# Performance work log

Measured on AMD Instinct MI355X. Metric: run time of the kernel, lower is better.

## Reference

```python
import math
import jax, jax.numpy as jnp
import numpy as np

NLAT, NLON = 61, 120
C, H = 64, 4
DH = C // H
HID = 128
NSEG = NLAT * NLON  # number of grid points / softmax segments
EPS = 1e-6
SCALE = 1.0 / math.sqrt(DH)


def _build_geometry():
    """Neighbor pairs within theta_cutoff on the equiangular (pole-including) grid.

    The neighborhood structure is longitude-shift invariant, so we enumerate it
    for output longitude 0 and replicate with a modular longitude shift.
    """
    nlat, nlon = NLAT, NLON
    theta = np.pi * np.arange(nlat) / (nlat - 1)           # colatitudes incl. poles
    lam = 2.0 * np.pi * np.arange(nlon) / nlon
    theta_cutoff = 7.0 / math.sqrt(math.pi) * math.pi / (nlat - 1)
    ct, st = np.cos(theta), np.sin(theta)
    # great-circle distance between (theta_o, 0) and (theta_i, dlon): [nlat, nlat, nlon]
    cosd = (ct[:, None, None] * ct[None, :, None]
            + st[:, None, None] * st[None, :, None] * np.cos(lam)[None, None, :])
    dist = np.arccos(np.clip(cosd, -1.0, 1.0))
    ho, hi, dl = np.nonzero(dist <= theta_cutoff)          # E reference-column entries
    wo = np.arange(nlon)
    out_idx = (ho[:, None] * nlon + wo[None, :]).reshape(-1).astype(np.int32)
    in_idx = (hi[:, None] * nlon + (dl[:, None] + wo[None, :]) % nlon).reshape(-1).astype(np.int32)
    # quadrature (integration) weights: sin(theta) measure, zero at the poles
    w = (st * (np.pi / (nlat - 1)) * (2.0 * np.pi / nlon)).astype(np.float32)
    quad_w = np.repeat(w, nlon)                            # [NSEG]
    return jnp.asarray(out_idx), jnp.asarray(in_idx), jnp.asarray(quad_w)


def setup_inputs() -> dict:
    key = jax.random.key(0)
    ks = jax.random.split(key, 8)
    out_idx, in_idx, quad_w = _build_geometry()

    def w(k, shape, fan_in):
        return jax.random.normal(k, shape, dtype=jnp.float32) / np.float32(np.sqrt(fan_in))

    return {
        "x": jax.random.normal(ks[0], (1, C, NLAT, NLON), dtype=jnp.float32),
        "wq": w(ks[1], (C, C), C),
        "wk": w(ks[2], (C, C), C),
        "wv": w(ks[3], (C, C), C),
        "wo": w(ks[4], (C, C), C),
        "w1": w(ks[5], (HID, C), C),
        "b1": jnp.zeros((HID,), jnp.float32),
        "w2": w(ks[6], (C, HID), HID),
        "b2": jnp.zeros((C,), jnp.float32),
        "ln0_g": jnp.ones((C,), jnp.float32),
        "ln0_b": jnp.zeros((C,), jnp.float32),
        "ln1_g": jnp.ones((C,), jnp.float32),
        "ln1_b": jnp.zeros((C,), jnp.float32),
        "quad_w": quad_w,
        "out_idx": out_idx,
        "in_idx": in_idx,
    }


def _layernorm(x, g, b):
    # channel-wise LayerNorm at every spatial location; x: [B, C, H, W]
    m = jnp.mean(x, axis=1, keepdims=True)
    v = jnp.mean((x - m) ** 2, axis=1, keepdims=True)
    xh = (x - m) * jax.lax.rsqrt(v + EPS)
    return xh * g[None, :, None, None] + b[None, :, None, None]


def _neighborhood_attn(x, wq, wk, wv, wo, quad_w, out_idx, in_idx):
    # x: [B, C, nlat, nlon] (fp32)
    B = x.shape[0]
    q = jnp.einsum('oc,bchw->bohw', wq, x).reshape(B, H, DH, NSEG)
    k = jnp.einsum('oc,bchw->bohw', wk, x).reshape(B, H, DH, NSEG)
    v = jnp.einsum('oc,bchw->bohw', wv, x).reshape(B, H, DH, NSEG)
    qg = q[..., out_idx]                                   # [B,H,DH,NNZ]
    kg = k[..., in_idx]
    s = jnp.einsum('bhdn,bhdn->bhn', qg, kg) * SCALE       # [B,H,NNZ]
    s = jnp.moveaxis(s, -1, 0)                             # [NNZ,B,H]
    smax = jax.ops.segment_max(s, out_idx, num_segments=NSEG)
    # quadrature-weighted, numerically stable softmax over each neighborhood
    alpha = jnp.exp(s - smax[out_idx]) * quad_w[in_idx][:, None, None]
    vg = jnp.moveaxis(v[..., in_idx], -1, 0)               # [NNZ,B,H,DH]
    num = jax.ops.segment_sum(alpha[..., None] * vg, out_idx, num_segments=NSEG)
    den = jax.ops.segment_sum(alpha, out_idx, num_segments=NSEG)
    att = num / den[..., None]                             # [NSEG,B,H,DH]
    att = jnp.moveaxis(att, 0, -1).reshape(B, C, NLAT, NLON)
    return jnp.einsum('oc,bchw->bohw', wo, att)


def reference(x, wq, wk, wv, wo, w1, b1, w2, b2, ln0_g, ln0_b, ln1_g, ln1_b,
              quad_w, out_idx, in_idx):
    residual = x
    h0 = _layernorm(x, ln0_g, ln0_b)
    a = _neighborhood_attn(h0.astype(jnp.float32), wq, wk, wv, wo,
                           quad_w, out_idx, in_idx).astype(x.dtype)
    x1 = a + residual
    h1 = _layernorm(x1, ln1_g, ln1_b)
    m = jax.nn.gelu(jnp.einsum('fc,bchw->bfhw', w1, h1) + b1[None, :, None, None],
                    approximate=False)
    m = jnp.einsum('cf,bfhw->bchw', w2, m) + b2[None, :, None, None]
    return m + x1
```

## Files before the change

### kernel.cpp

```cpp
#include <hip/hip_runtime.h>
#include <math.h>

#define NSEG 7320
#define NLON 120
#define HIDN 128
#define ECH  16
#define MAXCH 48

__global__ __launch_bounds__(64) void k1_ln_qkv(
    const float* __restrict__ x,  const float* __restrict__ wq,
    const float* __restrict__ wk, const float* __restrict__ wv,
    const float* __restrict__ g,  const float* __restrict__ b,
    const int* __restrict__ out_idx, const int* __restrict__ in_idx,
    const float* __restrict__ qw, int E,
    float* __restrict__ q_pl, float* __restrict__ k_pl, float* __restrict__ v_pl,
    int* __restrict__ row_start, int4* __restrict__ meta,
    float4* __restrict__ zbase)
{
    const int lane = threadIdx.x;
    const int tile = blockIdx.x;
    const int grp  = blockIdx.y;

    if (grp >= 25) {
        const int n4 = (68 * NSEG) / 4;
        for (int i = ((grp - 25) * 115 + tile) * 64 + lane; i < n4; i += 2 * 115 * 64)
            zbase[i] = make_float4(0.f, 0.f, 0.f, 0.f);
        return;
    }
    if (grp == 24) {
        for (int e = tile * 64 + lane; e < E; e += 115 * 64) {
            int ho = out_idx[e * NLON] / NLON;
            if (e == 0) {
                row_start[ho] = 0;
            } else {
                int hp = out_idx[(e - 1) * NLON] / NLON;
                if (hp != ho) row_start[ho] = e;
            }
            if (e == E - 1) row_start[ho + 1] = E;
            int i0 = in_idx[e * NLON];
            int hi = i0 / NLON;
            int dl = i0 - hi * NLON;
            meta[e] = make_int4(hi * NLON, dl, __float_as_int(qw[i0]), ho);
        }
        return;
    }

    const int n = tile * 64 + lane;
    if (n >= NSEG) return;

    float xv[64];
    float s = 0.f, s2 = 0.f;
#pragma unroll
    for (int c = 0; c < 64; ++c) { float t = x[c * NSEG + n]; xv[c] = t; s += t; s2 += t * t; }
    float mean = s * 0.015625f;
    float var  = s2 * 0.015625f - mean * mean;
    float rstd = rsqrtf(var + 1e-6f);
#pragma unroll
    for (int c = 0; c < 64; ++c) xv[c] = (xv[c] - mean) * rstd * g[c] + b[c];

    const int mm    = grp >> 3;
    const int obase = (grp & 7) * 8;
    const float* __restrict__ w = (mm == 0) ? wq : (mm == 1) ? wk : wv;
    float* __restrict__ dst = (mm == 0) ? q_pl : (mm == 1) ? k_pl : v_pl;
    const float scale = (mm == 0) ? 0.25f : 1.0f;

#pragma unroll
    for (int j = 0; j < 8; ++j) {
        int o = obase + j;
        float acc = 0.f;
#pragma unroll
        for (int c = 0; c < 64; ++c) acc += w[o * 64 + c] * xv[c];
        dst[o * NSEG + n] = acc * scale;
    }
}

__global__ __launch_bounds__(128) void k2_attn(
    const float* __restrict__ q_pl, const float* __restrict__ k_pl,
    const float* __restrict__ v_pl,
    const int4* __restrict__ meta,  const int* __restrict__ row_start,
    float* __restrict__ num, float* __restrict__ den)
{
    const int id   = blockIdx.x;
    const int ho   = (id & 7) + 8 * ((id >> 3) & 7);
    if (ho >= 61) return;
    const int ch   = id >> 6;
    const int head = ch & 3;
    const int cb   = head * 16;

    const int wo  = threadIdx.x;
    const bool aw = wo < NLON;
    const int woc = aw ? wo : (NLON - 1);

    int e0 = __builtin_amdgcn_readfirstlane(row_start[ho]);
    int e1 = __builtin_amdgcn_readfirstlane(row_start[ho + 1]);
    int eb = e0 + (ch >> 2) * ECH;
    if (eb >= e1) return;
    int ee = eb + ECH; if (ee > e1) ee = e1;

    const int segc = ho * NLON + woc;
    const float* __restrict__ qb = q_pl + (size_t)cb * NSEG;
    const float* __restrict__ kb = k_pl + (size_t)cb * NSEG;
    const float* __restrict__ vb = v_pl + (size_t)cb * NSEG;

    float qreg[16];
#pragma unroll
    for (int c = 0; c < 16; ++c) qreg[c] = qb[c * NSEG + segc];

    float acc[16];
#pragma unroll
    for (int c = 0; c < 16; ++c) acc[c] = 0.f;
    float dh = 0.f;

#pragma unroll 2
    for (int e = eb; e < ee; ++e) {
        int4 mt = meta[e];
        int dlw = mt.y + woc; if (dlw >= NLON) dlw -= NLON;
        const float* __restrict__ kp = kb + (mt.x + dlw);
        const float* __restrict__ vp = vb + (mt.x + dlw);

        float sa = 0.f, sb = 0.f;
#pragma unroll
        for (int c = 0; c < 8; ++c)  sa += qreg[c]     * kp[c * NSEG];
#pragma unroll
        for (int c = 0; c < 8; ++c)  sb += qreg[8 + c] * kp[(8 + c) * NSEG];

        float qwv = aw ? __int_as_float(mt.z) : 0.f;
        float a = __expf(sa + sb) * qwv;
        dh += a;

#pragma unroll
        for (int c = 0; c < 16; ++c) acc[c] = fmaf(a, vp[c * NSEG], acc[c]);
    }

    if (aw) {
        const int seg = ho * NLON + wo;
#pragma unroll
        for (int c = 0; c < 16; ++c) atomicAdd(&num[(cb + c) * NSEG + seg], acc[c]);
        atomicAdd(&den[head * NSEG + seg], dh);
    }
}

__global__ __launch_bounds__(64) void k23a_wo_mlp1(
    const float* __restrict__ num, const float* __restrict__ den,
    const float* __restrict__ wo,  const float* __restrict__ x,
    const float* __restrict__ w1,  const float* __restrict__ b1,
    const float* __restrict__ g1,  const float* __restrict__ bb1,
    float* __restrict__ x1, float* __restrict__ m_act)
{
    const int lane = threadIdx.x;
    const int n    = blockIdx.x * 64 + lane;
    if (n >= NSEG) return;

    float rdh[4];
#pragma unroll
    for (int h = 0; h < 4; ++h) rdh[h] = 1.0f / den[h * NSEG + n];

    float x1v[64];
#pragma unroll
    for (int o = 0; o < 64; ++o) x1v[o] = x[o * NSEG + n];

    for (int c = 0; c < 64; ++c) {
        float att = num[c * NSEG + n] * rdh[c >> 4];
        const float* __restrict__ wcol = wo + c;
#pragma unroll
        for (int o = 0; o < 64; ++o) x1v[o] = fmaf(wcol[o * 64], att, x1v[o]);
    }

    if (blockIdx.y == 0) {
#pragma unroll
        for (int o = 0; o < 64; ++o) x1[o * NSEG + n] = x1v[o];
    }

    float s = 0.f, s2 = 0.f;
#pragma unroll
    for (int o = 0; o < 64; ++o) { s += x1v[o]; s2 += x1v[o] * x1v[o]; }
    float mean = s * 0.015625f;
    float var  = s2 * 0.015625f - mean * mean;
    float rstd = rsqrtf(var + 1e-6f);

    const int h0 = blockIdx.y * 16;
    float mh[16];
#pragma unroll
    for (int j = 0; j < 16; ++j) mh[j] = b1[h0 + j];
    for (int c = 0; c < 64; ++c) {
        float xn = (x1v[c] - mean) * rstd * g1[c] + bb1[c];
        const float* __restrict__ w1c = w1 + h0 * 64 + c;
#pragma unroll
        for (int j = 0; j < 16; ++j) mh[j] = fmaf(w1c[j * 64], xn, mh[j]);
    }
#pragma unroll
    for (int j = 0; j < 16; ++j)
        m_act[(h0 + j) * NSEG + n] =
            0.5f * mh[j] * (1.0f + erff(mh[j] * 0.70710678118654752f));
}

__global__ __launch_bounds__(64) void k3b_mlp2(
    const float* __restrict__ m_act, const float* __restrict__ w2,
    const float* __restrict__ b2,    const float* __restrict__ x1,
    float* __restrict__ out)
{
    const int lane = threadIdx.x;
    const int n    = blockIdx.x * 64 + lane;
    if (n >= NSEG) return;
    const int c0   = blockIdx.y * 8;

    float acc[8];
#pragma unroll
    for (int j = 0; j < 8; ++j) acc[j] = 0.f;

#pragma unroll 8
    for (int h = 0; h < HIDN; ++h) {
        float mh = m_act[h * NSEG + n];
#pragma unroll
        for (int j = 0; j < 8; ++j) acc[j] += w2[(c0 + j) * HIDN + h] * mh;
    }
#pragma unroll
    for (int j = 0; j < 8; ++j) {
        int c = c0 + j;
        out[c * NSEG + n] = acc[j] + b2[c] + x1[c * NSEG + n];
    }
}

extern "C" void kernel_launch(void* const* d_in, const int* in_sizes, int n_in,
                              void* d_out, int out_size, void* d_ws, size_t ws_size,
                              hipStream_t stream)
{
    const float* x    = (const float*)d_in[0];
    const float* wq   = (const float*)d_in[1];
    const float* wk   = (const float*)d_in[2];
    const float* wv   = (const float*)d_in[3];
    const float* wo   = (const float*)d_in[4];
    const float* w1   = (const float*)d_in[5];
    const float* b1   = (const float*)d_in[6];
    const float* w2   = (const float*)d_in[7];
    const float* b2   = (const float*)d_in[8];
    const float* ln0g = (const float*)d_in[9];
    const float* ln0b = (const float*)d_in[10];
    const float* ln1g = (const float*)d_in[11];
    const float* ln1b = (const float*)d_in[12];
    const float* qw   = (const float*)d_in[13];
    const int* out_idx = (const int*)d_in[14];
    const int* in_idx  = (const int*)d_in[15];
    float* out = (float*)d_out;

    const int NNZ = in_sizes[15];
    const int E   = NNZ / NLON;
    const size_t N64 = (size_t)NSEG * 64;

    float* ws    = (float*)d_ws;
    float* q_pl  = ws;
    float* k_pl  = ws + N64;
    float* v_pl  = ws + 2 * N64;
    float* num   = ws + 3 * N64;
    float* den   = ws + 4 * N64;
    float* x1    = ws + 4 * N64 + 4 * NSEG;
    float* m_act = ws + 5 * N64 + 4 * NSEG;
    int*   row_start = (int*)(ws + 7 * N64 + 4 * NSEG);
    int4*  meta  = (int4*)(ws + 7 * N64 + 4 * NSEG + 64);

    hipLaunchKernelGGL(k1_ln_qkv, dim3(115, 27), dim3(64), 0, stream,
                       x, wq, wk, wv, ln0g, ln0b, out_idx, in_idx, qw, E,
                       q_pl, k_pl, v_pl, row_start, meta, (float4*)num);
    hipLaunchKernelGGL(k2_attn, dim3(64 * 192), dim3(128), 0, stream,
                       q_pl, k_pl, v_pl, meta, row_start, num, den);
    hipLaunchKernelGGL(k23a_wo_mlp1, dim3(115, 8), dim3(64), 0, stream,
                       num, den, wo, x, w1, b1, ln1g, ln1b, x1, m_act);
    hipLaunchKernelGGL(k3b_mlp2, dim3(115, 8), dim3(64), 0, stream,
                       m_act, w2, b2, x1, out);
}
```

Baseline: 227.2 us.

## Fuse all stages into one cooperative persistent kernel with grid syncs

Replaces the four separate launches with a single cooperative kernel of 512 blocks × 256 threads. The stages (LN+QKV, attention, output projection, LN1+MLP1, MLP2) are separated by grid.sync, and each stage walks its work items in a grid-stride loop. The output projection is split out of MLP1 into its own phase, so LN1 now re-reads x1 from memory for each hidden group. The aim is to remove inter-kernel launch gaps, at the cost of grid-wide barriers and much lower resident occupancy for the latency-bound gather-heavy attention phase.

```diff
diff --git a/kernel.cpp b/kernel.cpp
--- a/kernel.cpp
+++ b/kernel.cpp
@@ -1,223 +1,221 @@
 #include <hip/hip_runtime.h>
+#include <hip/hip_cooperative_groups.h>
 #include <math.h>
+
+namespace cg = cooperative_groups;
 
 #define NSEG 7320
 #define NLON 120
 #define HIDN 128
 #define ECH  16
-#define MAXCH 48
-
-__global__ __launch_bounds__(64) void k1_ln_qkv(
-    const float* __restrict__ x,  const float* __restrict__ wq,
-    const float* __restrict__ wk, const float* __restrict__ wv,
-    const float* __restrict__ g,  const float* __restrict__ b,
+#define NRCH 48
+#define NTILE 29
+
+__global__ __launch_bounds__(256, 2) void mega(
+    const float* __restrict__ x,
+    const float* __restrict__ wq, const float* __restrict__ wk,
+    const float* __restrict__ wv, const float* __restrict__ wo,
+    const float* __restrict__ w1, const float* __restrict__ b1,
+    const float* __restrict__ w2, const float* __restrict__ b2,
+    const float* __restrict__ ln0g, const float* __restrict__ ln0b,
+    const float* __restrict__ ln1g, const float* __restrict__ ln1b,
+    const float* __restrict__ qw,
     const int* __restrict__ out_idx, const int* __restrict__ in_idx,
-    const float* __restrict__ qw, int E,
+    int E,
     float* __restrict__ q_pl, float* __restrict__ k_pl, float* __restrict__ v_pl,
+    float* __restrict__ num,  float* __restrict__ den,
+    float* __restrict__ x1,   float* __restrict__ m_act,
     int* __restrict__ row_start, int4* __restrict__ meta,
-    float4* __restrict__ zbase)
-{
-    const int lane = threadIdx.x;
-    const int tile = blockIdx.x;
-    const int grp  = blockIdx.y;
-
-    if (grp >= 25) {
-        const int n4 = (68 * NSEG) / 4;
-        for (int i = ((grp - 25) * 115 + tile) * 64 + lane; i < n4; i += 2 * 115 * 64)
-            zbase[i] = make_float4(0.f, 0.f, 0.f, 0.f);
-        return;
-    }
-    if (grp == 24) {
-        for (int e = tile * 64 + lane; e < E; e += 115 * 64) {
-            int ho = out_idx[e * NLON] / NLON;
-            if (e == 0) {
-                row_start[ho] = 0;
-            } else {
-                int hp = out_idx[(e - 1) * NLON] / NLON;
-                if (hp != ho) row_start[ho] = e;
-            }
-            if (e == E - 1) row_start[ho + 1] = E;
-            int i0 = in_idx[e * NLON];
-            int hi = i0 / NLON;
-            int dl = i0 - hi * NLON;
-            meta[e] = make_int4(hi * NLON, dl, __float_as_int(qw[i0]), ho);
-        }
-        return;
-    }
-
-    const int n = tile * 64 + lane;
-    if (n >= NSEG) return;
-
-    float xv[64];
-    float s = 0.f, s2 = 0.f;
-#pragma unroll
-    for (int c = 0; c < 64; ++c) { float t = x[c * NSEG + n]; xv[c] = t; s += t; s2 += t * t; }
-    float mean = s * 0.015625f;
-    float var  = s2 * 0.015625f - mean * mean;
-    float rstd = rsqrtf(var + 1e-6f);
-#pragma unroll
-    for (int c = 0; c < 64; ++c) xv[c] = (xv[c] - mean) * rstd * g[c] + b[c];
-
-    const int mm    = grp >> 3;
-    const int obase = (grp & 7) * 8;
-    const float* __restrict__ w = (mm == 0) ? wq : (mm == 1) ? wk : wv;
-    float* __restrict__ dst = (mm == 0) ? q_pl : (mm == 1) ? k_pl : v_pl;
-    const float scale = (mm == 0) ? 0.25f : 1.0f;
-
-#pragma unroll
-    for (int j = 0; j < 8; ++j) {
-        int o = obase + j;
-        float acc = 0.f;
-#pragma unroll
-        for (int c = 0; c < 64; ++c) acc += w[o * 64 + c] * xv[c];
-        dst[o * NSEG + n] = acc * scale;
-    }
-}
-
-__global__ __launch_bounds__(128) void k2_attn(
-    const float* __restrict__ q_pl, const float* __restrict__ k_pl,
-    const float* __restrict__ v_pl,
-    const int4* __restrict__ meta,  const int* __restrict__ row_start,
-    float* __restrict__ num, float* __restrict__ den)
-{
-    const int id   = blockIdx.x;
-    const int ho   = (id & 7) + 8 * ((id >> 3) & 7);
-    if (ho >= 61) return;
-    const int ch   = id >> 6;
-    const int head = ch & 3;
-    const int cb   = head * 16;
-
-    const int wo  = threadIdx.x;
-    const bool aw = wo < NLON;
-    const int woc = aw ? wo : (NLON - 1);
-
-    int e0 = __builtin_amdgcn_readfirstlane(row_start[ho]);
-    int e1 = __builtin_amdgcn_readfirstlane(row_start[ho + 1]);
-    int eb = e0 + (ch >> 2) * ECH;
-    if (eb >= e1) return;
-    int ee = eb + ECH; if (ee > e1) ee = e1;
-
-    const int segc = ho * NLON + woc;
-    const float* __restrict__ qb = q_pl + (size_t)cb * NSEG;
-    const float* __restrict__ kb = k_pl + (size_t)cb * NSEG;
-    const float* __restrict__ vb = v_pl + (size_t)cb * NSEG;
-
-    float qreg[16];
-#pragma unroll
-    for (int c = 0; c < 16; ++c) qreg[c] = qb[c * NSEG + segc];
-
-    float acc[16];
-#pragma unroll
-    for (int c = 0; c < 16; ++c) acc[c] = 0.f;
-    float dh = 0.f;
-
-#pragma unroll 2
-    for (int e = eb; e < ee; ++e) {
-        int4 mt = meta[e];
-        int dlw = mt.y + woc; if (dlw >= NLON) dlw -= NLON;
-        const float* __restrict__ kp = kb + (mt.x + dlw);
-        const float* __restrict__ vp = vb + (mt.x + dlw);
-
-        float sa = 0.f, sb = 0.f;
-#pragma unroll
-        for (int c = 0; c < 8; ++c)  sa += qreg[c]     * kp[c * NSEG];
-#pragma unroll
-        for (int c = 0; c < 8; ++c)  sb += qreg[8 + c] * kp[(8 + c) * NSEG];
-
-        float qwv = aw ? __int_as_float(mt.z) : 0.f;
-        float a = __expf(sa + sb) * qwv;
-        dh += a;
-
-#pragma unroll
-        for (int c = 0; c < 16; ++c) acc[c] = fmaf(a, vp[c * NSEG], acc[c]);
-    }
-
-    if (aw) {
-        const int seg = ho * NLON + wo;
-#pragma unroll
-        for (int c = 0; c < 16; ++c) atomicAdd(&num[(cb + c) * NSEG + seg], acc[c]);
-        atomicAdd(&den[head * NSEG + seg], dh);
-    }
-}
-
-__global__ __launch_bounds__(64) void k23a_wo_mlp1(
-    const float* __restrict__ num, const float* __restrict__ den,
-    const float* __restrict__ wo,  const float* __restrict__ x,
-    const float* __restrict__ w1,  const float* __restrict__ b1,
-    const float* __restrict__ g1,  const float* __restrict__ bb1,
-    float* __restrict__ x1, float* __restrict__ m_act)
-{
-    const int lane = threadIdx.x;
-    const int n    = blockIdx.x * 64 + lane;
-    if (n >= NSEG) return;
-
-    float rdh[4];
-#pragma unroll
-    for (int h = 0; h < 4; ++h) rdh[h] = 1.0f / den[h * NSEG + n];
-
-    float x1v[64];
-#pragma unroll
-    for (int o = 0; o < 64; ++o) x1v[o] = x[o * NSEG + n];
-
-    for (int c = 0; c < 64; ++c) {
-        float att = num[c * NSEG + n] * rdh[c >> 4];
-        const float* __restrict__ wcol = wo + c;
-#pragma unroll
-        for (int o = 0; o < 64; ++o) x1v[o] = fmaf(wcol[o * 64], att, x1v[o]);
-    }
-
-    if (blockIdx.y == 0) {
-#pragma unroll
-        for (int o = 0; o < 64; ++o) x1[o * NSEG + n] = x1v[o];
-    }
-
-    float s = 0.f, s2 = 0.f;
-#pragma unroll
-    for (int o = 0; o < 64; ++o) { s += x1v[o]; s2 += x1v[o] * x1v[o]; }
-    float mean = s * 0.015625f;
-    float var  = s2 * 0.015625f - mean * mean;
-    float rstd = rsqrtf(var + 1e-6f);
-
-    const int h0 = blockIdx.y * 16;
-    float mh[16];
-#pragma unroll
-    for (int j = 0; j < 16; ++j) mh[j] = b1[h0 + j];
-    for (int c = 0; c < 64; ++c) {
-        float xn = (x1v[c] - mean) * rstd * g1[c] + bb1[c];
-        const float* __restrict__ w1c = w1 + h0 * 64 + c;
-#pragma unroll
-        for (int j = 0; j < 16; ++j) mh[j] = fmaf(w1c[j * 64], xn, mh[j]);
-    }
-#pragma unroll
-    for (int j = 0; j < 16; ++j)
-        m_act[(h0 + j) * NSEG + n] =
-            0.5f * mh[j] * (1.0f + erff(mh[j] * 0.70710678118654752f));
-}
-
-__global__ __launch_bounds__(64) void k3b_mlp2(
-    const float* __restrict__ m_act, const float* __restrict__ w2,
-    const float* __restrict__ b2,    const float* __restrict__ x1,
     float* __restrict__ out)
 {
-    const int lane = threadIdx.x;
-    const int n    = blockIdx.x * 64 + lane;
-    if (n >= NSEG) return;
-    const int c0   = blockIdx.y * 8;
-
-    float acc[8];
-#pragma unroll
-    for (int j = 0; j < 8; ++j) acc[j] = 0.f;
-
+    cg::grid_group grid = cg::this_grid();
+    const int tid = threadIdx.x;
+    const int nb  = gridDim.x;
+    const int gid = blockIdx.x * 256 + tid;
+    const int gsz = nb * 256;
+
+    {
+        float4* z = (float4*)num;
+        const int n4 = (68 * NSEG) / 4;
+        for (int i = gid; i < n4; i += gsz)
+            z[i] = make_float4(0.f, 0.f, 0.f, 0.f);
+    }
+    for (int e = gid; e < E; e += gsz) {
+        int ho = out_idx[e * NLON] / NLON;
+        if (e == 0) {
+            row_start[ho] = 0;
+        } else {
+            int hp = out_idx[(e - 1) * NLON] / NLON;
+            if (hp != ho) row_start[ho] = e;
+        }
+        if (e == E - 1) row_start[ho + 1] = E;
+        int i0 = in_idx[e * NLON];
+        int hi = i0 / NLON;
+        int dl = i0 - hi * NLON;
+        meta[e] = make_int4(hi * NLON, dl, __float_as_int(qw[i0]), ho);
+    }
+    for (int it = blockIdx.x; it < NTILE * 24; it += nb) {
+        int tile = it % NTILE, grp = it / NTILE;
+        int n = tile * 256 + tid;
+        bool act = n < NSEG;
+        int nn = act ? n : (NSEG - 1);
+
+        float s = 0.f, s2 = 0.f;
+        for (int c = 0; c < 64; ++c) { float t = x[c * NSEG + nn]; s += t; s2 += t * t; }
+        float mean = s * 0.015625f;
+        float var  = s2 * 0.015625f - mean * mean;
+        float r    = rsqrtf(var + 1e-6f);
+
+        int mm = grp >> 3, ob = (grp & 7) * 8;
+        const float* __restrict__ w = (mm == 0) ? wq : (mm == 1) ? wk : wv;
+        float* __restrict__ dst = (mm == 0) ? q_pl : (mm == 1) ? k_pl : v_pl;
+        float scale = (mm == 0) ? 0.25f : 1.0f;
+
+        float acc[8];
+#pragma unroll
+        for (int j = 0; j < 8; ++j) acc[j] = 0.f;
+        for (int c = 0; c < 64; ++c) {
+            float xh = (x[c * NSEG + nn] - mean) * r * ln0g[c] + ln0b[c];
+            const float* __restrict__ wc = w + ob * 64 + c;
+#pragma unroll
+            for (int j = 0; j < 8; ++j) acc[j] = fmaf(wc[j * 64], xh, acc[j]);
+        }
+        if (act)
+#pragma unroll
+            for (int j = 0; j < 8; ++j) dst[(ob + j) * NSEG + n] = acc[j] * scale;
+    }
+    grid.sync();
+
+    {
+        const int total = 61 * NRCH * 4;
+        const int sub = tid >> 7;
+        const int wol = tid & 127;
+        const bool aw = wol < NLON;
+        const int woc = aw ? wol : (NLON - 1);
+        for (int base = blockIdx.x * 2; base < total; base += nb * 2) {
+            int item = base + sub;
+            if (item >= total) continue;
+            int row  = item % 61;
+            int rest = item / 61;
+            int chunk = rest % NRCH;
+            int head  = rest / NRCH;
+            int e0 = __builtin_amdgcn_readfirstlane(row_start[row]);
+            int e1 = __builtin_amdgcn_readfirstlane(row_start[row + 1]);
+            int eb = e0 + chunk * ECH;
+            if (eb >= e1) continue;
+            int ee = eb + ECH; if (ee > e1) ee = e1;
+
+            const int cb = head * 16;
+            const int segc = row * NLON + woc;
+            const float* __restrict__ qb = q_pl + (size_t)cb * NSEG;
+            const float* __restrict__ kb = k_pl + (size_t)cb * NSEG;
+            const float* __restrict__ vb = v_pl + (size_t)cb * NSEG;
+
+            float qreg[16];
+#pragma unroll
+            for (int c = 0; c < 16; ++c) qreg[c] = qb[c * NSEG + segc];
+            float acc[16];
+#pragma unroll
+            for (int c = 0; c < 16; ++c) acc[c] = 0.f;
+            float dh = 0.f;
+
+#pragma unroll 2
+            for (int e = eb; e < ee; ++e) {
+                int4 mt = meta[e];
+                int dlw = mt.y + woc; if (dlw >= NLON) dlw -= NLON;
+                const float* __restrict__ kp = kb + (mt.x + dlw);
+                const float* __restrict__ vp = vb + (mt.x + dlw);
+                float sa = 0.f, sb = 0.f;
+#pragma unroll
+                for (int c = 0; c < 8; ++c) sa += qreg[c]     * kp[c * NSEG];
+#pragma unroll
+                for (int c = 0; c < 8; ++c) sb += qreg[8 + c] * kp[(8 + c) * NSEG];
+                float qwv = aw ? __int_as_float(mt.z) : 0.f;
+                float a = __expf(sa + sb) * qwv;
+                dh += a;
+#pragma unroll
+                for (int c = 0; c < 16; ++c) acc[c] = fmaf(a, vp[c * NSEG], acc[c]);
+            }
+            if (aw) {
+                const int seg = row * NLON + wol;
+#pragma unroll
+                for (int c = 0; c < 16; ++c)
+                    atomicAdd(&num[(cb + c) * NSEG + seg], acc[c]);
+                atomicAdd(&den[head * NSEG + seg], dh);
+            }
+        }
+    }
+    grid.sync();
+
+    for (int it = blockIdx.x; it < NTILE * 8; it += nb) {
+        int tile = it % NTILE, og = it / NTILE;
+        int n = tile * 256 + tid;
+        if (n >= NSEG) continue;
+        float rdh[4];
+#pragma unroll
+        for (int h = 0; h < 4; ++h) rdh[h] = 1.0f / den[h * NSEG + n];
+        const int o0 = og * 8;
+        float acc[8];
+#pragma unroll
+        for (int j = 0; j < 8; ++j) acc[j] = 0.f;
+        for (int c = 0; c < 64; ++c) {
+            float a = num[c * NSEG + n] * rdh[c >> 4];
+            const float* __restrict__ wc = wo + o0 * 64 + c;
+#pragma unroll
+            for (int j = 0; j < 8; ++j) acc[j] = fmaf(wc[j * 64], a, acc[j]);
+        }
+#pragma unroll
+        for (int j = 0; j < 8; ++j)
+            x1[(o0 + j) * NSEG + n] = acc[j] + x[(o0 + j) * NSEG + n];
+    }
+    grid.sync();
+
+    for (int it = blockIdx.x; it < NTILE * 8; it += nb) {
+        int tile = it % NTILE, hg = it / NTILE;
+        int n = tile * 256 + tid;
+        if (n >= NSEG) continue;
+        float s = 0.f, s2 = 0.f;
+        for (int c = 0; c < 64; ++c) { float t = x1[c * NSEG + n]; s += t; s2 += t * t; }
+        float mean = s * 0.015625f;
+        float var  = s2 * 0.015625f - mean * mean;
+        float r    = rsqrtf(var + 1e-6f);
+        const int h0 = hg * 16;
+        float mh[16];
+#pragma unroll
+        for (int j = 0; j < 16; ++j) mh[j] = b1[h0 + j];
+        for (int c = 0; c < 64; ++c) {
+            float xn = (x1[c * NSEG + n] - mean) * r * ln1g[c] + ln1b[c];
+            const float* __restrict__ wc = w1 + h0 * 64 + c;
+#pragma unroll
+            for (int j = 0; j < 16; ++j) mh[j] = fmaf(wc[j * 64], xn, mh[j]);
+        }
+#pragma unroll
+        for (int j = 0; j < 16; ++j)
+            m_act[(h0 + j) * NSEG + n] =
+                0.5f * mh[j] * (1.0f + erff(mh[j] * 0.70710678118654752f));
+    }
+    grid.sync();
+
+    for (int it = blockIdx.x; it < NTILE * 8; it += nb) {
+        int tile = it % NTILE, cgp = it / NTILE;
+        int n = tile * 256 + tid;
+        if (n >= NSEG) continue;
+        const int c0 = cgp * 8;
+        float acc[8];
+#pragma unroll
+        for (int j = 0; j < 8; ++j) acc[j] = 0.f;
 #pragma unroll 8
-    for (int h = 0; h < HIDN; ++h) {
-        float mh = m_act[h * NSEG + n];
-#pragma unroll
-        for (int j = 0; j < 8; ++j) acc[j] += w2[(c0 + j) * HIDN + h] * mh;
-    }
-#pragma unroll
-    for (int j = 0; j < 8; ++j) {
-        int c = c0 + j;
-        out[c * NSEG + n] = acc[j] + b2[c] + x1[c * NSEG + n];
+        for (int h = 0; h < HIDN; ++h) {
+            float mh = m_act[h * NSEG + n];
+            const float* __restrict__ wc = w2 + c0 * HIDN + h;
+#pragma unroll
+            for (int j = 0; j < 8; ++j) acc[j] = fmaf(wc[j * HIDN], mh, acc[j]);
+        }
+#pragma unroll
+        for (int j = 0; j < 8; ++j) {
+            int c = c0 + j;
+            out[c * NSEG + n] = acc[j] + b2[c] + x1[c * NSEG + n];
+        }
     }
 }
 
@@ -243,8 +241,7 @@
     const int* in_idx  = (const int*)d_in[15];
     float* out = (float*)d_out;
 
-    const int NNZ = in_sizes[15];
-    const int E   = NNZ / NLON;
+    int E = in_sizes[15] / NLON;
     const size_t N64 = (size_t)NSEG * 64;
 
     float* ws    = (float*)d_ws;
@@ -258,13 +255,15 @@
     int*   row_start = (int*)(ws + 7 * N64 + 4 * NSEG);
     int4*  meta  = (int4*)(ws + 7 * N64 + 4 * NSEG + 64);
 
-    hipLaunchKernelGGL(k1_ln_qkv, dim3(115, 27), dim3(64), 0, stream,
-                       x, wq, wk, wv, ln0g, ln0b, out_idx, in_idx, qw, E,
-                       q_pl, k_pl, v_pl, row_start, meta, (float4*)num);
-    hipLaunchKernelGGL(k2_attn, dim3(64 * 192), dim3(128), 0, stream,
-                       q_pl, k_pl, v_pl, meta, row_start, num, den);
-    hipLaunchKernelGGL(k23a_wo_mlp1, dim3(115, 8), dim3(64), 0, stream,
-                       num, den, wo, x, w1, b1, ln1g, ln1b, x1, m_act);
-    hipLaunchKernelGGL(k3b_mlp2, dim3(115, 8), dim3(64), 0, stream,
-                       m_act, w2, b2, x1, out);
+    void* args[] = {
+        (void*)&x, (void*)&wq, (void*)&wk, (void*)&wv, (void*)&wo,
+        (void*)&w1, (void*)&b1, (void*)&w2, (void*)&b2,
+        (void*)&ln0g, (void*)&ln0b, (void*)&ln1g, (void*)&ln1b,
+        (void*)&qw, (void*)&out_idx, (void*)&in_idx, (void*)&E,
+        (void*)&q_pl, (void*)&k_pl, (void*)&v_pl,
+        (void*)&num, (void*)&den, (void*)&x1, (void*)&m_act,
+        (void*)&row_start, (void*)&meta, (void*)&out
+    };
+    hipLaunchCooperativeKernel((const void*)mega, dim3(512), dim3(256),
+                               args, 0, stream);
 }
```

Result: slower. 458.6 us (+101.8%).
